# Performance work log

Hardware: AMD Instinct MI355X
Metric: run time of the kernel (lower is better)

Reference implementation:

```python
import jax, jax.numpy as jnp
import numpy as np

N, E, L, H, D_HID, D_IN, D_NEI, S_NEI, N_CLS = 30000, 480000, 2, 4, 128, 128, 64, 10, 2
HD = D_HID // H  # 32 per-head dim


def _mha(x, in_w, in_b, out_w, out_b, n_heads=4):
    # x: [N, S, D]; in_w: [D, 3D]; out_w: [D, D]
    n, s, d = x.shape
    hd = d // n_heads
    qkv = x @ in_w + in_b  # [N, S, 3D]
    q, k, v = jnp.split(qkv, 3, axis=-1)
    rs = lambda t: t.reshape(n, s, n_heads, hd).transpose(0, 2, 1, 3)  # [N,H,S,hd]
    q, k, v = rs(q), rs(k), rs(v)
    attn = jax.nn.softmax(jnp.einsum('nhqd,nhkd->nhqk', q, k) / np.sqrt(hd).astype(np.float32), axis=-1)
    o = jnp.einsum('nhqk,nhkd->nhqd', attn, v).transpose(0, 2, 1, 3).reshape(n, s, d)
    return o @ out_w + out_b


def _layer_norm(x, g, b, eps=1e-5):
    m = jnp.mean(x, axis=-1, keepdims=True)
    v = jnp.var(x, axis=-1, keepdims=True)
    return (x - m) * jax.lax.rsqrt(v + eps) * g + b


def _transformer_conv(src, dst, h, wq_i, bq_i, wk_i, bk_i, wv_i, bv_i):
    # per-head graph transformer conv: q from dst, k/v from src, edge softmax over dst
    q = (h @ wq_i + bq_i).reshape(N, H, HD)
    k = (h @ wk_i + bk_i).reshape(N, H, HD)
    v = (h @ wv_i + bv_i).reshape(N, H, HD)
    score = jnp.sum(q[dst] * k[src], axis=-1) / np.sqrt(HD).astype(np.float32)  # [E, H]
    smax = jax.ops.segment_max(score, dst, num_segments=N)  # [N, H]
    ex = jnp.exp(score - smax[dst])  # [E, H]
    denom = jax.ops.segment_sum(ex, dst, num_segments=N)  # [N, H]
    num = jax.ops.segment_sum(ex[:, :, None] * v[src], dst, num_segments=N)  # [N, H, HD]
    out = num / jnp.maximum(denom, 1e-9)[:, :, None]
    return out.reshape(N, D_HID)


def setup_inputs() -> dict:
    key = jax.random.key(0)
    ks = jax.random.split(key, 24)
    d = {}
    d['x'] = jax.random.normal(ks[0], (N, D_IN), jnp.float32)
    d['nei_features'] = jax.random.normal(ks[1], (N, S_NEI, D_NEI), jnp.float32)
    d['edge_index'] = jax.random.randint(ks[2], (L, 2, E), 0, N, jnp.int32)
    sc = 0.05
    d['w_in'] = jax.random.normal(ks[3], (D_IN, D_HID), jnp.float32) * sc
    d['b_in'] = jax.random.normal(ks[4], (D_HID,), jnp.float32) * sc
    d['mha_in_w'] = jax.random.normal(ks[5], (D_NEI, 3 * D_NEI), jnp.float32) * sc
    d['mha_in_b'] = jax.random.normal(ks[6], (3 * D_NEI,), jnp.float32) * sc
    d['mha_out_w'] = jax.random.normal(ks[7], (D_NEI, D_NEI), jnp.float32) * sc
    d['mha_out_b'] = jax.random.normal(ks[8], (D_NEI,), jnp.float32) * sc
    d['w_nei'] = jax.random.normal(ks[9], (D_NEI, D_HID), jnp.float32) * sc
    d['b_nei'] = jax.random.normal(ks[10], (D_HID,), jnp.float32) * sc
    d['wq'] = jax.random.normal(ks[11], (L, D_HID, D_HID), jnp.float32) * sc
    d['bq'] = jax.random.normal(ks[12], (L, D_HID), jnp.float32) * sc
    d['wk'] = jax.random.normal(ks[13], (L, D_HID, D_HID), jnp.float32) * sc
    d['bk'] = jax.random.normal(ks[14], (L, D_HID), jnp.float32) * sc
    d['wv'] = jax.random.normal(ks[15], (L, D_HID, D_HID), jnp.float32) * sc
    d['bv'] = jax.random.normal(ks[16], (L, D_HID), jnp.float32) * sc
    d['ln_g'] = jnp.ones((L, D_HID), jnp.float32)
    d['ln_b'] = jnp.zeros((L, D_HID), jnp.float32)
    d['w_out'] = jax.random.normal(ks[17], (D_HID, N_CLS), jnp.float32) * sc
    d['b_out'] = jnp.zeros((N_CLS,), jnp.float32)
    return d


def reference(x, nei_features, edge_index, w_in, b_in, mha_in_w, mha_in_b,
              mha_out_w, mha_out_b, w_nei, b_nei, wq, bq, wk, bk, wv, bv,
              ln_g, ln_b, w_out, b_out):
    h = x @ w_in + b_in  # input_proj
    # neighbor-feature self-attention branch (nn.MultiheadAttention, eval mode)
    nei = _mha(nei_features, mha_in_w, mha_in_b, mha_out_w, mha_out_b).mean(axis=1)
    h = h + (nei @ w_nei + b_nei)
    for i in range(L):
        src, dst = edge_index[i, 0], edge_index[i, 1]
        h = _transformer_conv(src, dst, h, wq[i], bq[i], wk[i], bk[i], wv[i], bv[i])
        h = jax.nn.relu(h)
        h = _layer_norm(h, ln_g[i], ln_b[i])
        # dropout is identity in eval mode
    return h @ w_out + b_out
```

## Files before the change

### kernel.cpp

```cpp
#include <hip/hip_runtime.h>
#include <hip/hip_bf16.h>

#define NN 30000
#define EE 480000

typedef __attribute__((ext_vector_type(8))) short short8;
typedef __attribute__((ext_vector_type(4))) short short4v;
typedef __attribute__((ext_vector_type(4))) float floatx4;
typedef unsigned short u16;

__device__ __forceinline__ u16 f2bf(float f) {
  union { float f; unsigned u; } v; v.f = f;
  unsigned u = v.u;
  u += 0x7FFFu + ((u >> 16) & 1u);
  return (u16)(u >> 16);
}
__device__ __forceinline__ float bf2f(u16 u) {
  union { unsigned u; float f; } v; v.u = ((unsigned)u) << 16;
  return v.f;
}
__device__ __forceinline__ float bflo(unsigned u) {
  union { unsigned x; float f; } v; v.x = u << 16; return v.f;
}
__device__ __forceinline__ float bfhi(unsigned u) {
  union { unsigned x; float f; } v; v.x = u & 0xFFFF0000u; return v.f;
}
__device__ __forceinline__ unsigned packbf(float a, float b) {
  return (unsigned)f2bf(a) | ((unsigned)f2bf(b) << 16);
}
__device__ __forceinline__ short8 pack8(float4 A, float4 B) {
  union { unsigned u[4]; short8 s; } r;
  r.u[0] = packbf(A.x, A.y);
  r.u[1] = packbf(A.z, A.w);
  r.u[2] = packbf(B.x, B.y);
  r.u[3] = packbf(B.z, B.w);
  return r.s;
}

template <int CTRL>
__device__ __forceinline__ float dppadd(float v) {
  int s = __builtin_amdgcn_update_dpp(0, __builtin_bit_cast(int, v), CTRL, 0xF, 0xF, true);
  return v + __builtin_bit_cast(float, s);
}
__device__ __forceinline__ float rowsum16(float v) {
  v = dppadd<0x121>(v); v = dppadd<0x122>(v); v = dppadd<0x124>(v); v = dppadd<0x128>(v);
  return v;
}
__device__ __forceinline__ float rowsum8(float v) {
  v = dppadd<0xB1>(v); v = dppadd<0x4E>(v); v = dppadd<0x141>(v);
  return v;
}

#define MFMA32 __builtin_amdgcn_mfma_f32_16x16x32_bf16

#if __has_builtin(__builtin_amdgcn_mfma_f32_16x16x16bf16_1k)
__device__ __forceinline__ floatx4 MFMA16(short4v a, short4v b, floatx4 c) {
  return __builtin_amdgcn_mfma_f32_16x16x16bf16_1k(a, b, c, 0, 0, 0);
}
#else
__device__ __forceinline__ floatx4 MFMA16(short4v a, short4v b, floatx4 c) {
  asm volatile("v_mfma_f32_16x16x16_bf16 %0, %1, %2, %0"
               : "+v"(c) : "v"(a), "v"(b));
  return c;
}
#endif

__global__ __launch_bounds__(128) void k_fuse(
    const float* __restrict__ out_w, const float* __restrict__ out_b,
    const float* __restrict__ w_nei, const float* __restrict__ b_nei,
    const float* __restrict__ b_in,
    float* __restrict__ fusedW, float* __restrict__ fusedB) {
  int i = blockIdx.x, j = threadIdx.x;
  if (i < 64) {
    float a = 0.f;
    for (int kk = 0; kk < 64; ++kk) a = fmaf(out_w[i * 64 + kk], w_nei[kk * 128 + j], a);
    fusedW[i * 128 + j] = a;
  } else {
    float a = b_in[j] + b_nei[j];
    for (int kk = 0; kk < 64; ++kk) a = fmaf(out_b[kk], w_nei[kk * 128 + j], a);
    fusedB[j] = a;
  }
}

__global__ __launch_bounds__(128) void k_prepB(
    const float* __restrict__ in_w, const float* __restrict__ fusedW,
    const float* __restrict__ fusedB, const float* __restrict__ in_b,
    float* __restrict__ G, float* __restrict__ fusedB2) {
  int bx = blockIdx.x, c = threadIdx.x;
  if (bx < 256) {
    int h = bx >> 6, d = bx & 63;
    float a = 0.f;
    for (int dd = 0; dd < 16; ++dd)
      a = fmaf(in_w[d * 192 + 128 + h * 16 + dd], fusedW[(h * 16 + dd) * 128 + c], a);
    G[bx * 128 + c] = a;
  } else {
    float a = fusedB[c];
    for (int d = 0; d < 64; ++d) a = fmaf(in_b[128 + d], fusedW[d * 128 + c], a);
    fusedB2[c] = a;
  }
}

__global__ __launch_bounds__(128) void k_prep2(
    const float* __restrict__ w_in, const float* __restrict__ G,
    const float* __restrict__ wq, const float* __restrict__ wk,
    const float* __restrict__ wv, const float* __restrict__ in_w,
    u16* __restrict__ wtP2, u16* __restrict__ wt3, u16* __restrict__ wtQK) {
  int bx = blockIdx.x, t = threadIdx.x;
  if (bx < 128) {
    int c = bx;
#pragma unroll
    for (int part = 0; part < 3; ++part) {
      int k = part * 128 + t;
      float v = (k < 128) ? w_in[(size_t)k * 128 + c] : G[(size_t)(k - 128) * 128 + c];
      wtP2[(size_t)c * 384 + k] = f2bf(v);
    }
  } else if (bx < 896) {
    int b2 = bx - 128;
    int l = b2 / 384, rem = b2 % 384, o = rem >> 7, c = rem & 127;
    const float* w = (o == 0 ? wq : (o == 1 ? wk : wv)) + (size_t)l * 16384;
    wt3[(size_t)b2 * 128 + t] = f2bf(w[(size_t)t * 128 + c]);
  } else {
    int c = (bx - 896) * 2 + (t >> 6), kk = t & 63;
    float s = (c < 64) ? 0.25f : 1.f;
    wtQK[(size_t)c * 64 + kk] = f2bf(s * in_w[(size_t)kk * 192 + c]);
  }
}

__global__ __launch_bounds__(640) void k_mha8(
    const float* __restrict__ xn,
    const u16* __restrict__ wtQK,
    const float* __restrict__ in_b,
    u16* __restrict__ Yb) {
  __shared__ unsigned qks[112 * 66];
  __shared__ float cs_lds[10][4][12];
  int t = threadIdx.x, w = t >> 6, l = t & 63;
  int lr = l & 15, lq = l >> 4;
  const floatx4 zf = {0.f, 0.f, 0.f, 0.f};
  size_t r0 = (size_t)blockIdx.x * 100;

  if (w < 7) {
    int row = w * 16 + lr;
    size_t arow = r0 + row;
    if (arow > 299999) arow = 299999;
    const float* xp = xn + arow * 64 + lq * 8;
    float4 f0 = *(const float4*)xp;
    float4 f1 = *(const float4*)(xp + 4);
    float4 f2 = *(const float4*)(xp + 32);
    float4 f3 = *(const float4*)(xp + 36);
    short8 a0 = pack8(f0, f1), a1 = pack8(f2, f3);
    floatx4 acc[8];
#pragma unroll
    for (int ct = 0; ct < 8; ++ct) acc[ct] = zf;
#pragma unroll
    for (int ct = 0; ct < 8; ++ct) {
      const short8* bp = (const short8*)(wtQK + (size_t)(ct * 16 + lr) * 64);
      acc[ct] = MFMA32(a0, bp[lq], acc[ct], 0, 0, 0);
      acc[ct] = MFMA32(a1, bp[4 + lq], acc[ct], 0, 0, 0);
    }
#pragma unroll
    for (int ct = 0; ct < 4; ++ct) {
      float bq_ = in_b[ct * 16 + lr] * 0.25f;
      float bk_ = in_b[64 + ct * 16 + lr];
#pragma unroll
      for (int r = 0; r < 4; ++r)
        qks[(w * 16 + lq * 4 + r) * 66 + ct * 16 + lr] =
            packbf(acc[ct][r] + bq_, acc[ct + 4][r] + bk_);
    }
  }
  __syncthreads();

  int seqc = lr < 10 ? lr : 9;
  {
#pragma unroll
    for (int h = 0; h < 4; ++h) {
      const unsigned* rp = &qks[(w * 10 + seqc) * 66 + h * 16 + lq * 4];
      uint2 u0 = *(const uint2*)rp;
      uint2 u1 = *(const uint2*)(rp + 2);
      union { unsigned u[2]; short4v s; } qv, kv;
      qv.u[0] = (u0.x & 0xFFFFu) | (u0.y << 16);
      qv.u[1] = (u1.x & 0xFFFFu) | (u1.y << 16);
      kv.u[0] = (u0.x >> 16) | (u0.y & 0xFFFF0000u);
      kv.u[1] = (u1.x >> 16) | (u1.y & 0xFFFF0000u);
      floatx4 s4 = MFMA16(kv.s, qv.s, zf);
      int j0 = lq * 4;
      float e0 = (j0 + 0 < 10) ? __expf(s4[0]) : 0.f;
      float e1 = (j0 + 1 < 10) ? __expf(s4[1]) : 0.f;
      float e2 = (j0 + 2 < 10) ? __expf(s4[2]) : 0.f;
      float e3 = (j0 + 3 < 10) ? __expf(s4[3]) : 0.f;
      float den = e0 + e1 + e2 + e3;
      den += __shfl_xor(den, 16, 64);
      den += __shfl_xor(den, 32, 64);
      float rden = 0.1f / den;
      float v0 = (lr < 10) ? e0 * rden : 0.f;
      float v1 = (lr < 10) ? e1 * rden : 0.f;
      float v2 = (lr < 10) ? e2 * rden : 0.f;
      float v3 = (lr < 10) ? e3 * rden : 0.f;
      v0 = rowsum16(v0);
      v1 = rowsum16(v1);
      v2 = rowsum16(v2);
      v3 = rowsum16(v3);
      if (lr == 0) {
        cs_lds[w][h][lq * 4 + 0] = v0;
        cs_lds[w][h][lq * 4 + 1] = v1;
        cs_lds[w][h][lq * 4 + 2] = v2;
        cs_lds[w][h][lq * 4 + 3] = v3;
      }
    }
    size_t node = (size_t)blockIdx.x * 10 + w;
    const float* xp2 = xn + node * 640 + l;
    float y0 = 0.f, y1 = 0.f, y2 = 0.f, y3 = 0.f;
#pragma unroll
    for (int j = 0; j < 10; ++j) {
      float xv = xp2[j * 64];
      y0 = fmaf(cs_lds[w][0][j], xv, y0);
      y1 = fmaf(cs_lds[w][1][j], xv, y1);
      y2 = fmaf(cs_lds[w][2][j], xv, y2);
      y3 = fmaf(cs_lds[w][3][j], xv, y3);
    }
    size_t yb = node * 256;
    Yb[yb + l] = f2bf(y0);
    Yb[yb + 64 + l] = f2bf(y1);
    Yb[yb + 128 + l] = f2bf(y2);
    Yb[yb + 192 + l] = f2bf(y3);
  }
}

__global__ __launch_bounds__(256) void k_projqkv(
    const float* __restrict__ x, const u16* __restrict__ Yb,
    const u16* __restrict__ wtP2, const float* __restrict__ fusedB2,
    const u16* __restrict__ wt3l,
    const float* __restrict__ bqL, const float* __restrict__ bkL,
    const float* __restrict__ bvL,
    unsigned* __restrict__ q2, unsigned* __restrict__ k2, unsigned* __restrict__ v2) {
  __shared__ u16 hs[64 * 128];
  int t = threadIdx.x, w = t >> 6, l = t & 63, lr = l & 15, lq = l >> 4;
  int row0 = blockIdx.x * 64 + w * 16;
  int arow = row0 + lr; if (arow >= NN) arow = NN - 1;
  {
    const float* xp = x + (size_t)arow * 128;
    const short8* yp = (const short8*)(Yb + (size_t)arow * 256);
    short8 afr[12];
#pragma unroll
    for (int kb = 0; kb < 4; ++kb) {
      float4 fa = *(const float4*)(xp + kb * 32 + lq * 8);
      float4 fb = *(const float4*)(xp + kb * 32 + lq * 8 + 4);
      afr[kb] = pack8(fa, fb);
    }
#pragma unroll
    for (int m = 0; m < 8; ++m) afr[4 + m] = yp[m * 4 + lq];
    floatx4 acc[8];
#pragma unroll
    for (int ct = 0; ct < 8; ++ct) acc[ct] = (floatx4){0.f, 0.f, 0.f, 0.f};
#pragma unroll
    for (int ct = 0; ct < 8; ++ct) {
      const short8* bp = (const short8*)(wtP2 + (size_t)(ct * 16 + lr) * 384);
#pragma unroll
      for (int kb = 0; kb < 12; ++kb)
        acc[ct] = MFMA32(afr[kb], bp[kb * 4 + lq], acc[ct], 0, 0, 0);
    }
    int lrow = w * 16;
#pragma unroll
    for (int ct = 0; ct < 8; ++ct) {
      int col = ct * 16 + lr;
      float bias = fusedB2[col];
#pragma unroll
      for (int r = 0; r < 4; ++r)
        hs[(lrow + lq * 4 + r) * 128 + col] = f2bf(acc[ct][r] + bias);
    }
  }
  __syncthreads();
  {
    int lrow = w * 16 + lr;
    const short8* ap = (const short8*)(hs + lrow * 128);
    short8 a0 = ap[lq], a1 = ap[4 + lq], a2 = ap[8 + lq], a3 = ap[12 + lq];
    const short8* wt8 = (const short8*)wt3l;
    floatx4 acc[24];
#pragma unroll
    for (int ct = 0; ct < 24; ++ct) acc[ct] = (floatx4){0.f, 0.f, 0.f, 0.f};
#pragma unroll
    for (int ct = 0; ct < 24; ++ct) {
      const short8* bp = wt8 + (size_t)((ct >> 3) * 128 + (ct & 7) * 16 + lr) * 16;
      acc[ct] = MFMA32(a0, bp[lq], acc[ct], 0, 0, 0);
      acc[ct] = MFMA32(a1, bp[4 + lq], acc[ct], 0, 0, 0);
      acc[ct] = MFMA32(a2, bp[8 + lq], acc[ct], 0, 0, 0);
      acc[ct] = MFMA32(a3, bp[12 + lq], acc[ct], 0, 0, 0);
    }
#pragma unroll
    for (int o = 0; o < 3; ++o) {
      unsigned* op = o == 0 ? q2 : (o == 1 ? k2 : v2);
      const float* bp2 = o == 0 ? bqL : (o == 1 ? bkL : bvL);
#pragma unroll
      for (int cc = 0; cc < 4; ++cc) {
        int col = cc * 16 + lr;
        float blo = bp2[col], bhi = bp2[64 + col];
        floatx4 alo = acc[o * 8 + cc], ahi = acc[o * 8 + cc + 4];
#pragma unroll
        for (int r = 0; r < 4; ++r) {
          int row = row0 + lq * 4 + r;
          if (row < NN)
            op[(size_t)row * 64 + col] = packbf(alo[r] + blo, ahi[r] + bhi);
        }
      }
    }
  }
}

__global__ __launch_bounds__(256) void k_qkv4(
    const u16* __restrict__ hb, const u16* __restrict__ wt3l,
    const float* __restrict__ bqL, const float* __restrict__ bkL,
    const float* __restrict__ bvL,
    unsigned* __restrict__ q2, unsigned* __restrict__ k2, unsigned* __restrict__ v2) {
  int t = threadIdx.x, w = t >> 6, l = t & 63, lr = l & 15, lq = l >> 4;
  int row0 = blockIdx.x * 64 + w * 16;
  int arow = row0 + lr; if (arow >= NN) arow = NN - 1;
  const short8* ap = (const short8*)(hb + (size_t)arow * 128);
  short8 a0 = ap[lq], a1 = ap[4 + lq], a2 = ap[8 + lq], a3 = ap[12 + lq];
  const short8* wt8 = (const short8*)wt3l;
  floatx4 acc[24];
#pragma unroll
  for (int ct = 0; ct < 24; ++ct) acc[ct] = (floatx4){0.f, 0.f, 0.f, 0.f};
#pragma unroll
  for (int ct = 0; ct < 24; ++ct) {
    const short8* bp = wt8 + (size_t)((ct >> 3) * 128 + (ct & 7) * 16 + lr) * 16;
    acc[ct] = MFMA32(a0, bp[lq], acc[ct], 0, 0, 0);
    acc[ct] = MFMA32(a1, bp[4 + lq], acc[ct], 0, 0, 0);
    acc[ct] = MFMA32(a2, bp[8 + lq], acc[ct], 0, 0, 0);
    acc[ct] = MFMA32(a3, bp[12 + lq], acc[ct], 0, 0, 0);
  }
#pragma unroll
  for (int o = 0; o < 3; ++o) {
    unsigned* op = o == 0 ? q2 : (o == 1 ? k2 : v2);
    const float* bp2 = o == 0 ? bqL : (o == 1 ? bkL : bvL);
#pragma unroll
    for (int cc = 0; cc < 4; ++cc) {
      int col = cc * 16 + lr;
      float blo = bp2[col], bhi = bp2[64 + col];
      floatx4 alo = acc[o * 8 + cc], ahi = acc[o * 8 + cc + 4];
#pragma unroll
      for (int r = 0; r < 4; ++r) {
        int row = row0 + lq * 4 + r;
        if (row < NN)
          op[(size_t)row * 64 + col] = packbf(alo[r] + blo, ahi[r] + bhi);
      }
    }
  }
}

__global__ __launch_bounds__(256) void k_fill(const int* __restrict__ ei,
                                              int* __restrict__ cnt,
                                              int* __restrict__ esrc) {
  int gthr = blockIdx.x * 256 + threadIdx.x;
  if (gthr < 2 * EE) {
    int l = gthr >= EE;
    int e = gthr - l * EE;
    int s = ei[(size_t)(2 * l) * EE + e];
    int d = ei[(size_t)(2 * l + 1) * EE + e];
    int c = atomicAdd(&cnt[l * NN + d], 1);
    if (c < 64) esrc[((size_t)l * NN + d) * 64 + c] = s;
  }
}

__global__ __launch_bounds__(256) void k_sagg7(
    const unsigned* __restrict__ q2, const unsigned* __restrict__ k2,
    const unsigned* __restrict__ v2, const int* __restrict__ esrc,
    const int* __restrict__ cnt, const float* __restrict__ g,
    const float* __restrict__ bb, u16* __restrict__ hb,
    const float* __restrict__ wo, const float* __restrict__ bo,
    float* __restrict__ outp) {
  const float SC = 0.17677669529663687f;
  int t = threadIdx.x, w = t >> 6, l = t & 63;
  int e = l >> 4, dd = l & 15;
  int n = blockIdx.x * 4 + w;
  int deg = cnt[n]; if (deg > 64) deg = 64;
  const int* sp = esrc + (size_t)n * 64;
  uint4 qp = *(const uint4*)(q2 + (size_t)n * 64 + dd * 4);
  float ql0 = bflo(qp.x), ql1 = bflo(qp.y), ql2 = bflo(qp.z), ql3 = bflo(qp.w);
  float qh0 = bfhi(qp.x), qh1 = bfhi(qp.y), qh2 = bfhi(qp.z), qh3 = bfhi(qp.w);
  float dA0 = 0.f, dA1 = 0.f, dB0 = 0.f, dB1 = 0.f;
  float alA0 = 0.f, alA1 = 0.f, alA2 = 0.f, alA3 = 0.f;
  float ahA0 = 0.f, ahA1 = 0.f, ahA2 = 0.f, ahA3 = 0.f;
  float alB0 = 0.f, alB1 = 0.f, alB2 = 0.f, alB3 = 0.f;
  float ahB0 = 0.f, ahB1 = 0.f, ahB2 = 0.f, ahB3 = 0.f;
  uint4 kA = {0, 0, 0, 0}, vA = {0, 0, 0, 0};
  uint4 kB = {0, 0, 0, 0}, vB = {0, 0, 0, 0};
  bool mA = false, mB = false;
  if (deg > 0) {
    int iA = e < deg ? e : deg - 1;           mA = e < deg;
    int iB = 4 + e < deg ? 4 + e : deg - 1;   mB = 4 + e < deg;
    int sA = sp[iA], sB = sp[iB];
    kA = *(const uint4*)(k2 + (size_t)sA * 64 + dd * 4);
    vA = *(const uint4*)(v2 + (size_t)sA * 64 + dd * 4);
    kB = *(const uint4*)(k2 + (size_t)sB * 64 + dd * 4);
    vB = *(const uint4*)(v2 + (size_t)sB * 64 + dd * 4);
  }
  for (int base = 0; base < deg; base += 8) {
    uint4 kAn = {0, 0, 0, 0}, vAn = {0, 0, 0, 0};
    uint4 kBn = {0, 0, 0, 0}, vBn = {0, 0, 0, 0};
    bool mAn = false, mBn = false;
    int nb = base + 8;
    if (nb < deg) {
      int iA = nb + e < deg ? nb + e : deg - 1;         mAn = nb + e < deg;
      int iB = nb + 4 + e < deg ? nb + 4 + e : deg - 1; mBn = nb + 4 + e < deg;
      int sA = sp[iA], sB = sp[iB];
      kAn = *(const uint4*)(k2 + (size_t)sA * 64 + dd * 4);
      vAn = *(const uint4*)(v2 + (size_t)sA * 64 + dd * 4);
      kBn = *(const uint4*)(k2 + (size_t)sB * 64 + dd * 4);
      vBn = *(const uint4*)(v2 + (size_t)sB * 64 + dd * 4);
    }
    float rA0 = ql0 * bflo(kA.x) + ql1 * bflo(kA.y) + ql2 * bflo(kA.z) + ql3 * bflo(kA.w);
    float rA1 = qh0 * bfhi(kA.x) + qh1 * bfhi(kA.y) + qh2 * bfhi(kA.z) + qh3 * bfhi(kA.w);
    float rB0 = ql0 * bflo(kB.x) + ql1 * bflo(kB.y) + ql2 * bflo(kB.z) + ql3 * bflo(kB.w);
    float rB1 = qh0 * bfhi(kB.x) + qh1 * bfhi(kB.y) + qh2 * bfhi(kB.z) + qh3 * bfhi(kB.w);
    rA0 = rowsum8(rA0); rA1 = rowsum8(rA1);
    rB0 = rowsum8(rB0); rB1 = rowsum8(rB1);
    float pA0 = mA ? __expf(rA0 * SC) : 0.f;
    float pA1 = mA ? __expf(rA1 * SC) : 0.f;
    float pB0 = mB ? __expf(rB0 * SC) : 0.f;
    float pB1 = mB ? __expf(rB1 * SC) : 0.f;
    dA0 += pA0; dA1 += pA1; dB0 += pB0; dB1 += pB1;
    alA0 = fmaf(pA0, bflo(vA.x), alA0); alA1 = fmaf(pA0, bflo(vA.y), alA1);
    alA2 = fmaf(pA0, bflo(vA.z), alA2); alA3 = fmaf(pA0, bflo(vA.w), alA3);
    ahA0 = fmaf(pA1, bfhi(vA.x), ahA0); ahA1 = fmaf(pA1, bfhi(vA.y), ahA1);
    ahA2 = fmaf(pA1, bfhi(vA.z), ahA2); ahA3 = fmaf(pA1, bfhi(vA.w), ahA3);
    alB0 = fmaf(pB0, bflo(vB.x), alB0); alB1 = fmaf(pB0, bflo(vB.y), alB1);
    alB2 = fmaf(pB0, bflo(vB.z), alB2); alB3 = fmaf(pB0, bflo(vB.w), alB3);
    ahB0 = fmaf(pB1, bfhi(vB.x), ahB0); ahB1 = fmaf(pB1, bfhi(vB.y), ahB1);
    ahB2 = fmaf(pB1, bfhi(vB.z), ahB2); ahB3 = fmaf(pB1, bfhi(vB.w), ahB3);
    kA = kAn; vA = vAn; mA = mAn;
    kB = kBn; vB = vBn; mB = mBn;
  }
  float d0 = dA0 + dB0, d1 = dA1 + dB1;
  float al0 = alA0 + alB0, al1 = alA1 + alB1, al2 = alA2 + alB2, al3 = alA3 + alB3;
  float ah0 = ahA0 + ahB0, ah1 = ahA1 + ahB1, ah2 = ahA2 + ahB2, ah3 = ahA3 + ahB3;
  d0 += __shfl_xor(d0, 16, 64); d0 += __shfl_xor(d0, 32, 64);
  d1 += __shfl_xor(d1, 16, 64); d1 += __shfl_xor(d1, 32, 64);
  al0 += __shfl_xor(al0, 16, 64); al0 += __shfl_xor(al0, 32, 64);
  al1 += __shfl_xor(al1, 16, 64); al1 += __shfl_xor(al1, 32, 64);
  al2 += __shfl_xor(al2, 16, 64); al2 += __shfl_xor(al2, 32, 64);
  al3 += __shfl_xor(al3, 16, 64); al3 += __shfl_xor(al3, 32, 64);
  ah0 += __shfl_xor(ah0, 16, 64); ah0 += __shfl_xor(ah0, 32, 64);
  ah1 += __shfl_xor(ah1, 16, 64); ah1 += __shfl_xor(ah1, 32, 64);
  ah2 += __shfl_xor(ah2, 16, 64); ah2 += __shfl_xor(ah2, 32, 64);
  ah3 += __shfl_xor(ah3, 16, 64); ah3 += __shfl_xor(ah3, 32, 64);
  float rd0 = 1.f / fmaxf(d0, 1e-9f), rd1 = 1.f / fmaxf(d1, 1e-9f);
  float ol0 = fmaxf(al0 * rd0, 0.f), ol1 = fmaxf(al1 * rd0, 0.f);
  float ol2 = fmaxf(al2 * rd0, 0.f), ol3 = fmaxf(al3 * rd0, 0.f);
  float oh0 = fmaxf(ah0 * rd1, 0.f), oh1 = fmaxf(ah1 * rd1, 0.f);
  float oh2 = fmaxf(ah2 * rd1, 0.f), oh3 = fmaxf(ah3 * rd1, 0.f);
  float s1 = ol0 + ol1 + ol2 + ol3 + oh0 + oh1 + oh2 + oh3;
  float s2 = ol0 * ol0 + ol1 * ol1 + ol2 * ol2 + ol3 * ol3 +
             oh0 * oh0 + oh1 * oh1 + oh2 * oh2 + oh3 * oh3;
  s1 = rowsum16(s1);
  s2 = rowsum16(s2);
  float mean = s1 * (1.f / 128.f);
  float var = s2 * (1.f / 128.f) - mean * mean;
  float rs = rsqrtf(var + 1e-5f);
  if (e == 0) {
    floatx4 gl = *(const floatx4*)(g + dd * 4);
    floatx4 bl = *(const floatx4*)(bb + dd * 4);
    floatx4 gh = *(const floatx4*)(g + 64 + dd * 4);
    floatx4 bh = *(const floatx4*)(bb + 64 + dd * 4);
    float hl0 = (ol0 - mean) * rs * gl[0] + bl[0];
    float hl1 = (ol1 - mean) * rs * gl[1] + bl[1];
    float hl2 = (ol2 - mean) * rs * gl[2] + bl[2];
    float hl3 = (ol3 - mean) * rs * gl[3] + bl[3];
    float hh0 = (oh0 - mean) * rs * gh[0] + bh[0];
    float hh1 = (oh1 - mean) * rs * gh[1] + bh[1];
    float hh2 = (oh2 - mean) * rs * gh[2] + bh[2];
    float hh3 = (oh3 - mean) * rs * gh[3] + bh[3];
    if (outp == nullptr) {
      uint2 w0, w1;
      w0.x = packbf(hl0, hl1); w0.y = packbf(hl2, hl3);
      w1.x = packbf(hh0, hh1); w1.y = packbf(hh2, hh3);
      *(uint2*)(hb + (size_t)n * 128 + dd * 4) = w0;
      *(uint2*)(hb + (size_t)n * 128 + 64 + dd * 4) = w1;
    } else {
      const float2* wo2 = (const float2*)wo;
      float2 wa0 = wo2[dd * 4], wa1 = wo2[dd * 4 + 1];
      float2 wa2 = wo2[dd * 4 + 2], wa3 = wo2[dd * 4 + 3];
      float2 wb0 = wo2[64 + dd * 4], wb1 = wo2[64 + dd * 4 + 1];
      float2 wb2 = wo2[64 + dd * 4 + 2], wb3 = wo2[64 + dd * 4 + 3];
      float p0 = hl0 * wa0.x + hl1 * wa1.x + hl2 * wa2.x + hl3 * wa3.x +
                 hh0 * wb0.x + hh1 * wb1.x + hh2 * wb2.x + hh3 * wb3.x;
      float p1 = hl0 * wa0.y + hl1 * wa1.y + hl2 * wa2.y + hl3 * wa3.y +
                 hh0 * wb0.y + hh1 * wb1.y + hh2 * wb2.y + hh3 * wb3.y;
      p0 = rowsum16(p0);
      p1 = rowsum16(p1);
      if (dd == 0) {
        outp[n * 2] = p0 + bo[0];
        outp[n * 2 + 1] = p1 + bo[1];
      }
    }
  }
}

extern "C" void kernel_launch(void* const* d_in, const int* in_sizes, int n_in,
                              void* d_out, int out_size, void* d_ws, size_t ws_size,
                              hipStream_t stream) {
  const float* x = (const float*)d_in[0];
  const float* neif = (const float*)d_in[1];
  const int* ei = (const int*)d_in[2];
  const float* w_in = (const float*)d_in[3];
  const float* b_in = (const float*)d_in[4];
  const float* mha_in_w = (const float*)d_in[5];
  const float* mha_in_b = (const float*)d_in[6];
  const float* mha_out_w = (const float*)d_in[7];
  const float* mha_out_b = (const float*)d_in[8];
  const float* w_nei = (const float*)d_in[9];
  const float* b_nei = (const float*)d_in[10];
  const float* wq = (const float*)d_in[11];
  const float* bq = (const float*)d_in[12];
  const float* wk = (const float*)d_in[13];
  const float* bk = (const float*)d_in[14];
  const float* wv = (const float*)d_in[15];
  const float* bv = (const float*)d_in[16];
  const float* ln_g = (const float*)d_in[17];
  const float* ln_b = (const float*)d_in[18];
  const float* w_out = (const float*)d_in[19];
  const float* b_out = (const float*)d_in[20];
  float* out = (float*)d_out;

  char* wsb = (char*)d_ws;
  size_t off = 0;
  unsigned* q2 = (unsigned*)(wsb + off); off += (size_t)NN * 64 * 4;
  unsigned* k2 = (unsigned*)(wsb + off); off += (size_t)NN * 64 * 4;
  unsigned* v2 = (unsigned*)(wsb + off); off += (size_t)NN * 64 * 4;
  int* esrc = (int*)(wsb + off);         off += (size_t)2 * NN * 64 * 4;
  u16* Yb = (u16*)(wsb + off);           off += (size_t)NN * 256 * 2;
  u16* hb = (u16*)(wsb + off);           off += (size_t)NN * 128 * 2;
  u16* wt3 = (u16*)(wsb + off);          off += (size_t)768 * 128 * 2;
  u16* wtP2 = (u16*)(wsb + off);         off += (size_t)128 * 384 * 2;
  u16* wtQK = (u16*)(wsb + off);         off += (size_t)128 * 64 * 2;
  float* G = (float*)(wsb + off);        off += (size_t)256 * 128 * 4;
  float* fusedW = (float*)(wsb + off);   off += 64 * 128 * 4;
  float* fusedB = (float*)(wsb + off);   off += 128 * 4;
  float* fusedB2 = (float*)(wsb + off);  off += 128 * 4;
  int* cnt = (int*)(wsb + off);          off += (size_t)2 * NN * 4;

  k_fuse<<<65, 128, 0, stream>>>(mha_out_w, mha_out_b, w_nei, b_nei, b_in, fusedW, fusedB);
  k_prepB<<<257, 128, 0, stream>>>(mha_in_w, fusedW, fusedB, mha_in_b, G, fusedB2);
  k_prep2<<<960, 128, 0, stream>>>(w_in, G, wq, wk, wv, mha_in_w, wtP2, wt3, wtQK);

  k_mha8<<<3000, 640, 0, stream>>>(neif, wtQK, mha_in_b, Yb);

  hipMemsetAsync(cnt, 0, 2 * NN * sizeof(int), stream);
  k_fill<<<3750, 256, 0, stream>>>(ei, cnt, esrc);

  k_projqkv<<<469, 256, 0, stream>>>(x, Yb, wtP2, fusedB2, wt3,
                                     bq, bk, bv, q2, k2, v2);
  k_sagg7<<<NN / 4, 256, 0, stream>>>(q2, k2, v2, esrc, cnt,
                                      ln_g, ln_b, hb, w_out, b_out, nullptr);
  k_qkv4<<<469, 256, 0, stream>>>(hb, wt3 + (size_t)3 * 128 * 128,
                                  bq + 128, bk + 128, bv + 128, q2, k2, v2);
  k_sagg7<<<NN / 4, 256, 0, stream>>>(q2, k2, v2, esrc + (size_t)NN * 64,
                                      cnt + NN, ln_g + 128, ln_b + 128, hb,
                                      w_out, b_out, out);
}
```

Before: 300.0 us.

## Zero-fill edge lists and unroll aggregation to 16 edges per iteration

The aggregation kernel now takes four edges per lane group per iteration instead of two. It issues the index and K/V gathers for the first 16 edges before reading the degree, and it drops the deg-1 clamping by relying on a zeroed edge list, so padding entries point at node 0. Memset and fill now cover the esrc and cnt buffers together and run first in the stream. The aim is more memory-level parallelism, with more gathers in flight, at the cost of dropping the software prefetch of the next block. Padded slots still load node-0 data, which adds wasted loads for low-degree nodes.

```diff
diff --git a/kernel.cpp b/kernel.cpp
--- a/kernel.cpp
+++ b/kernel.cpp
@@ -360,7 +360,7 @@
   }
 }
 
-__global__ __launch_bounds__(256) void k_sagg7(
+__global__ __launch_bounds__(256) void k_sagg8(
     const unsigned* __restrict__ q2, const unsigned* __restrict__ k2,
     const unsigned* __restrict__ v2, const int* __restrict__ esrc,
     const int* __restrict__ cnt, const float* __restrict__ g,
@@ -371,67 +371,65 @@
   int t = threadIdx.x, w = t >> 6, l = t & 63;
   int e = l >> 4, dd = l & 15;
   int n = blockIdx.x * 4 + w;
+  const int* sp = esrc + (size_t)n * 64;
+  int si0 = sp[e], si1 = sp[4 + e], si2 = sp[8 + e], si3 = sp[12 + e];
+  uint4 qp = *(const uint4*)(q2 + (size_t)n * 64 + dd * 4);
   int deg = cnt[n]; if (deg > 64) deg = 64;
-  const int* sp = esrc + (size_t)n * 64;
-  uint4 qp = *(const uint4*)(q2 + (size_t)n * 64 + dd * 4);
+  uint4 kk0 = *(const uint4*)(k2 + (size_t)si0 * 64 + dd * 4);
+  uint4 vv0 = *(const uint4*)(v2 + (size_t)si0 * 64 + dd * 4);
+  uint4 kk1 = *(const uint4*)(k2 + (size_t)si1 * 64 + dd * 4);
+  uint4 vv1 = *(const uint4*)(v2 + (size_t)si1 * 64 + dd * 4);
+  uint4 kk2 = *(const uint4*)(k2 + (size_t)si2 * 64 + dd * 4);
+  uint4 vv2 = *(const uint4*)(v2 + (size_t)si2 * 64 + dd * 4);
+  uint4 kk3 = *(const uint4*)(k2 + (size_t)si3 * 64 + dd * 4);
+  uint4 vv3 = *(const uint4*)(v2 + (size_t)si3 * 64 + dd * 4);
+
   float ql0 = bflo(qp.x), ql1 = bflo(qp.y), ql2 = bflo(qp.z), ql3 = bflo(qp.w);
   float qh0 = bfhi(qp.x), qh1 = bfhi(qp.y), qh2 = bfhi(qp.z), qh3 = bfhi(qp.w);
-  float dA0 = 0.f, dA1 = 0.f, dB0 = 0.f, dB1 = 0.f;
-  float alA0 = 0.f, alA1 = 0.f, alA2 = 0.f, alA3 = 0.f;
-  float ahA0 = 0.f, ahA1 = 0.f, ahA2 = 0.f, ahA3 = 0.f;
-  float alB0 = 0.f, alB1 = 0.f, alB2 = 0.f, alB3 = 0.f;
-  float ahB0 = 0.f, ahB1 = 0.f, ahB2 = 0.f, ahB3 = 0.f;
-  uint4 kA = {0, 0, 0, 0}, vA = {0, 0, 0, 0};
-  uint4 kB = {0, 0, 0, 0}, vB = {0, 0, 0, 0};
-  bool mA = false, mB = false;
-  if (deg > 0) {
-    int iA = e < deg ? e : deg - 1;           mA = e < deg;
-    int iB = 4 + e < deg ? 4 + e : deg - 1;   mB = 4 + e < deg;
-    int sA = sp[iA], sB = sp[iB];
-    kA = *(const uint4*)(k2 + (size_t)sA * 64 + dd * 4);
-    vA = *(const uint4*)(v2 + (size_t)sA * 64 + dd * 4);
-    kB = *(const uint4*)(k2 + (size_t)sB * 64 + dd * 4);
-    vB = *(const uint4*)(v2 + (size_t)sB * 64 + dd * 4);
-  }
-  for (int base = 0; base < deg; base += 8) {
-    uint4 kAn = {0, 0, 0, 0}, vAn = {0, 0, 0, 0};
-    uint4 kBn = {0, 0, 0, 0}, vBn = {0, 0, 0, 0};
-    bool mAn = false, mBn = false;
-    int nb = base + 8;
-    if (nb < deg) {
-      int iA = nb + e < deg ? nb + e : deg - 1;         mAn = nb + e < deg;
-      int iB = nb + 4 + e < deg ? nb + 4 + e : deg - 1; mBn = nb + 4 + e < deg;
-      int sA = sp[iA], sB = sp[iB];
-      kAn = *(const uint4*)(k2 + (size_t)sA * 64 + dd * 4);
-      vAn = *(const uint4*)(v2 + (size_t)sA * 64 + dd * 4);
-      kBn = *(const uint4*)(k2 + (size_t)sB * 64 + dd * 4);
-      vBn = *(const uint4*)(v2 + (size_t)sB * 64 + dd * 4);
-    }
-    float rA0 = ql0 * bflo(kA.x) + ql1 * bflo(kA.y) + ql2 * bflo(kA.z) + ql3 * bflo(kA.w);
-    float rA1 = qh0 * bfhi(kA.x) + qh1 * bfhi(kA.y) + qh2 * bfhi(kA.z) + qh3 * bfhi(kA.w);
-    float rB0 = ql0 * bflo(kB.x) + ql1 * bflo(kB.y) + ql2 * bflo(kB.z) + ql3 * bflo(kB.w);
-    float rB1 = qh0 * bfhi(kB.x) + qh1 * bfhi(kB.y) + qh2 * bfhi(kB.z) + qh3 * bfhi(kB.w);
-    rA0 = rowsum8(rA0); rA1 = rowsum8(rA1);
-    rB0 = rowsum8(rB0); rB1 = rowsum8(rB1);
-    float pA0 = mA ? __expf(rA0 * SC) : 0.f;
-    float pA1 = mA ? __expf(rA1 * SC) : 0.f;
-    float pB0 = mB ? __expf(rB0 * SC) : 0.f;
-    float pB1 = mB ? __expf(rB1 * SC) : 0.f;
-    dA0 += pA0; dA1 += pA1; dB0 += pB0; dB1 += pB1;
-    alA0 = fmaf(pA0, bflo(vA.x), alA0); alA1 = fmaf(pA0, bflo(vA.y), alA1);
-    alA2 = fmaf(pA0, bflo(vA.z), alA2); alA3 = fmaf(pA0, bflo(vA.w), alA3);
-    ahA0 = fmaf(pA1, bfhi(vA.x), ahA0); ahA1 = fmaf(pA1, bfhi(vA.y), ahA1);
-    ahA2 = fmaf(pA1, bfhi(vA.z), ahA2); ahA3 = fmaf(pA1, bfhi(vA.w), ahA3);
-    alB0 = fmaf(pB0, bflo(vB.x), alB0); alB1 = fmaf(pB0, bflo(vB.y), alB1);
-    alB2 = fmaf(pB0, bflo(vB.z), alB2); alB3 = fmaf(pB0, bflo(vB.w), alB3);
-    ahB0 = fmaf(pB1, bfhi(vB.x), ahB0); ahB1 = fmaf(pB1, bfhi(vB.y), ahB1);
-    ahB2 = fmaf(pB1, bfhi(vB.z), ahB2); ahB3 = fmaf(pB1, bfhi(vB.w), ahB3);
-    kA = kAn; vA = vAn; mA = mAn;
-    kB = kBn; vB = vBn; mB = mBn;
-  }
-  float d0 = dA0 + dB0, d1 = dA1 + dB1;
-  float al0 = alA0 + alB0, al1 = alA1 + alB1, al2 = alA2 + alB2, al3 = alA3 + alB3;
-  float ah0 = ahA0 + ahB0, ah1 = ahA1 + ahB1, ah2 = ahA2 + ahB2, ah3 = ahA3 + ahB3;
+  float d0 = 0.f, d1 = 0.f;
+  float al0 = 0.f, al1 = 0.f, al2 = 0.f, al3 = 0.f;
+  float ah0 = 0.f, ah1 = 0.f, ah2 = 0.f, ah3 = 0.f;
+
+#define DOEDGE(KK, VV, VALID)                                                  \
+  {                                                                            \
+    float r0 = ql0 * bflo(KK.x) + ql1 * bflo(KK.y) + ql2 * bflo(KK.z) +        \
+               ql3 * bflo(KK.w);                                               \
+    float r1 = qh0 * bfhi(KK.x) + qh1 * bfhi(KK.y) + qh2 * bfhi(KK.z) +        \
+               qh3 * bfhi(KK.w);                                               \
+    r0 = rowsum8(r0);                                                          \
+    r1 = rowsum8(r1);                                                          \
+    float p0 = (VALID) ? __expf(r0 * SC) : 0.f;                                \
+    float p1 = (VALID) ? __expf(r1 * SC) : 0.f;                                \
+    d0 += p0; d1 += p1;                                                        \
+    al0 = fmaf(p0, bflo(VV.x), al0); al1 = fmaf(p0, bflo(VV.y), al1);          \
+    al2 = fmaf(p0, bflo(VV.z), al2); al3 = fmaf(p0, bflo(VV.w), al3);          \
+    ah0 = fmaf(p1, bfhi(VV.x), ah0); ah1 = fmaf(p1, bfhi(VV.y), ah1);          \
+    ah2 = fmaf(p1, bfhi(VV.z), ah2); ah3 = fmaf(p1, bfhi(VV.w), ah3);          \
+  }
+
+  DOEDGE(kk0, vv0, e < deg)
+  DOEDGE(kk1, vv1, 4 + e < deg)
+  DOEDGE(kk2, vv2, 8 + e < deg)
+  DOEDGE(kk3, vv3, 12 + e < deg)
+
+  for (int base = 16; base < deg; base += 16) {
+    int ti0 = sp[base + e], ti1 = sp[base + 4 + e];
+    int ti2 = sp[base + 8 + e], ti3 = sp[base + 12 + e];
+    kk0 = *(const uint4*)(k2 + (size_t)ti0 * 64 + dd * 4);
+    vv0 = *(const uint4*)(v2 + (size_t)ti0 * 64 + dd * 4);
+    kk1 = *(const uint4*)(k2 + (size_t)ti1 * 64 + dd * 4);
+    vv1 = *(const uint4*)(v2 + (size_t)ti1 * 64 + dd * 4);
+    kk2 = *(const uint4*)(k2 + (size_t)ti2 * 64 + dd * 4);
+    vv2 = *(const uint4*)(v2 + (size_t)ti2 * 64 + dd * 4);
+    kk3 = *(const uint4*)(k2 + (size_t)ti3 * 64 + dd * 4);
+    vv3 = *(const uint4*)(v2 + (size_t)ti3 * 64 + dd * 4);
+    DOEDGE(kk0, vv0, base + e < deg)
+    DOEDGE(kk1, vv1, base + 4 + e < deg)
+    DOEDGE(kk2, vv2, base + 8 + e < deg)
+    DOEDGE(kk3, vv3, base + 12 + e < deg)
+  }
+#undef DOEDGE
+
   d0 += __shfl_xor(d0, 16, 64); d0 += __shfl_xor(d0, 32, 64);
   d1 += __shfl_xor(d1, 16, 64); d1 += __shfl_xor(d1, 32, 64);
   al0 += __shfl_xor(al0, 16, 64); al0 += __shfl_xor(al0, 32, 64);
@@ -526,6 +524,7 @@
   unsigned* k2 = (unsigned*)(wsb + off); off += (size_t)NN * 64 * 4;
   unsigned* v2 = (unsigned*)(wsb + off); off += (size_t)NN * 64 * 4;
   int* esrc = (int*)(wsb + off);         off += (size_t)2 * NN * 64 * 4;
+  int* cnt = (int*)(wsb + off);          off += (size_t)2 * NN * 4;
   u16* Yb = (u16*)(wsb + off);           off += (size_t)NN * 256 * 2;
   u16* hb = (u16*)(wsb + off);           off += (size_t)NN * 128 * 2;
   u16* wt3 = (u16*)(wsb + off);          off += (size_t)768 * 128 * 2;
@@ -535,7 +534,9 @@
   float* fusedW = (float*)(wsb + off);   off += 64 * 128 * 4;
   float* fusedB = (float*)(wsb + off);   off += 128 * 4;
   float* fusedB2 = (float*)(wsb + off);  off += 128 * 4;
-  int* cnt = (int*)(wsb + off);          off += (size_t)2 * NN * 4;
+
+  hipMemsetAsync(esrc, 0, ((size_t)2 * NN * 64 + 2 * NN) * sizeof(int), stream);
+  k_fill<<<3750, 256, 0, stream>>>(ei, cnt, esrc);
 
   k_fuse<<<65, 128, 0, stream>>>(mha_out_w, mha_out_b, w_nei, b_nei, b_in, fusedW, fusedB);
   k_prepB<<<257, 128, 0, stream>>>(mha_in_w, fusedW, fusedB, mha_in_b, G, fusedB2);
@@ -543,16 +544,13 @@
 
   k_mha8<<<3000, 640, 0, stream>>>(neif, wtQK, mha_in_b, Yb);
 
-  hipMemsetAsync(cnt, 0, 2 * NN * sizeof(int), stream);
-  k_fill<<<3750, 256, 0, stream>>>(ei, cnt, esrc);
-
   k_projqkv<<<469, 256, 0, stream>>>(x, Yb, wtP2, fusedB2, wt3,
                                      bq, bk, bv, q2, k2, v2);
-  k_sagg7<<<NN / 4, 256, 0, stream>>>(q2, k2, v2, esrc, cnt,
+  k_sagg8<<<NN / 4, 256, 0, stream>>>(q2, k2, v2, esrc, cnt,
                                       ln_g, ln_b, hb, w_out, b_out, nullptr);
   k_qkv4<<<469, 256, 0, stream>>>(hb, wt3 + (size_t)3 * 128 * 128,
                                   bq + 128, bk + 128, bv + 128, q2, k2, v2);
-  k_sagg7<<<NN / 4, 256, 0, stream>>>(q2, k2, v2, esrc + (size_t)NN * 64,
+  k_sagg8<<<NN / 4, 256, 0, stream>>>(q2, k2, v2, esrc + (size_t)NN * 64,
                                       cnt + NN, ln_g + 128, ln_b + 128, hb,
                                       w_out, b_out, out);
 }
```

Result: no change. 305.6 us (+1.9%).
